# Kernel optimization log

Measured on AMD Instinct MI355X. Metric: run time of the kernel, lower is better.

Reference implementation:

```python
import jax, jax.numpy as jnp
import numpy as np

HEADS, KDIM, VDIM = 8, 32, 64  # ImageLinearAttention defaults
EPS = 1e-8

def lrelu(x):
    return jax.nn.leaky_relu(x, 0.2)

def up2(x):
    # torch nn.Upsample(scale_factor=2, mode='bilinear', align_corners=False)
    b, c, h, w = x.shape
    return jax.image.resize(x, (b, c, 2 * h, 2 * w), method='bilinear')

def blur(x):
    # normalized [1,2,1] outer-product depthwise blur (kornia filter2d, normalized=True)
    c = x.shape[1]
    f = jnp.array([1.0, 2.0, 1.0], dtype=x.dtype)
    k = (f[:, None] * f[None, :]) / 16.0
    kern = jnp.broadcast_to(k, (c, 1, 3, 3))
    return jax.lax.conv_general_dilated(x, kern, (1, 1), [(1, 1), (1, 1)], feature_group_count=c)

def conv2dmod(x, W, y, demod):
    # x [b,ci,h,w], W [co,ci,k,k], y [b,ci]; per-sample modulated (de)conv
    w = W[None] * (y[:, None, :, None, None] + 1.0)  # [b,co,ci,k,k]
    if demod:
        d = jax.lax.rsqrt(jnp.sum(w * w, axis=(2, 3, 4), keepdims=True) + EPS)
        w = w * d
    pad = (W.shape[-1] - 1) // 2  # same padding, stride=1, dilation=1
    conv1 = lambda xi, wi: jax.lax.conv_general_dilated(xi[None], wi, (1, 1), [(pad, pad), (pad, pad)])[0]
    return jax.vmap(conv1)(x, w)

def attn_and_ff(x, qw, kw, vw, ow, ob, ga, f1w, f1b, f2w, f2b, gf):
    # Residual(Rezero(ImageLinearAttention)) then Residual(Rezero(conv1x1-leaky-conv1x1))
    b, c, h, w = x.shape
    n = h * w
    xf = x.reshape(b, c, n)
    scale = KDIM ** -0.25
    q = (jnp.einsum('dc,bcn->bdn', qw, xf) * scale).reshape(b, HEADS, KDIM, n)
    k = (jnp.einsum('dc,bcn->bdn', kw, xf) * scale).reshape(b, HEADS, KDIM, n)
    v = jnp.einsum('dc,bcn->bdn', vw, xf).reshape(b, HEADS, VDIM, n)
    k = jax.nn.softmax(k, axis=-1)          # over pixels
    q = jax.nn.softmax(q, axis=-2)          # norm_queries: over key dim
    ctx = jnp.einsum('bhdn,bhen->bhde', k, v)
    out = jnp.einsum('bhdn,bhde->bhen', q, ctx).reshape(b, HEADS * VDIM, n)
    out = jnp.einsum('cd,bdn->bcn', ow, out) + ob[None, :, None]
    x = x + ga * out.reshape(b, c, h, w)
    h1 = lrelu(jnp.einsum('dc,bcn->bdn', f1w, x.reshape(b, c, n)) + f1b[None, :, None])
    ff = jnp.einsum('cd,bdn->bcn', f2w, h1) + f2b[None, :, None]
    return x + gf * ff.reshape(b, c, h, w)

def setup_inputs() -> dict:
    key = jax.random.key(0)
    ks = jax.random.split(key, 20)
    B, CIN, F, L, H, W = 4, 128, 64, 512, 64, 64
    DK, DV = HEADS * KDIM, HEADS * VDIM
    d = {}
    d['x'] = jax.random.normal(ks[0], (B, CIN, H, W), jnp.float32)
    d['prev_rgb'] = jax.random.normal(ks[1], (B, 3, 2 * H, 2 * W), jnp.float32)
    d['istyle'] = jax.random.normal(ks[2], (B, L), jnp.float32)
    d['noise1'] = jax.random.normal(ks[3], (B, F, 2 * H, 2 * W), jnp.float32)
    d['noise2'] = jax.random.normal(ks[4], (B, F, 2 * H, 2 * W), jnp.float32)
    d['conv1_w'] = jax.random.normal(ks[5], (F, CIN, 3, 3), jnp.float32) * (2.0 / (CIN * 9)) ** 0.5
    d['conv2_w'] = jax.random.normal(ks[6], (F, F, 3, 3), jnp.float32) * (2.0 / (F * 9)) ** 0.5
    d['style_w'] = jax.random.normal(ks[7], (F, L), jnp.float32) * L ** -0.5
    d['style_b'] = jnp.zeros((F,), jnp.float32)
    d['rgb_w'] = jax.random.normal(ks[8], (3, F, 1, 1), jnp.float32) * (2.0 / F) ** 0.5
    d['qw'] = jax.random.normal(ks[9], (2, DK, F), jnp.float32) * F ** -0.5
    d['kw'] = jax.random.normal(ks[10], (2, DK, F), jnp.float32) * F ** -0.5
    d['vw'] = jax.random.normal(ks[11], (2, DV, F), jnp.float32) * F ** -0.5
    d['ow'] = jax.random.normal(ks[12], (2, F, DV), jnp.float32) * DV ** -0.5
    d['ob'] = jnp.zeros((2, F), jnp.float32)
    d['ga'] = 0.1 * jnp.ones((2,), jnp.float32)  # rezero gate (nonzero for a meaningful baseline)
    d['f1w'] = jax.random.normal(ks[13], (2, 2 * F, F), jnp.float32) * F ** -0.5
    d['f1b'] = jnp.zeros((2, 2 * F), jnp.float32)
    d['f2w'] = jax.random.normal(ks[14], (2, F, 2 * F), jnp.float32) * (2 * F) ** -0.5
    d['f2b'] = jnp.zeros((2, F), jnp.float32)
    d['gf'] = 0.1 * jnp.ones((2,), jnp.float32)
    return d

def reference(x, prev_rgb, istyle, noise1, noise2, conv1_w, conv2_w, style_w, style_b, rgb_w,
              qw, kw, vw, ow, ob, ga, f1w, f1b, f2w, f2b, gf):
    b = x.shape[0]
    x = up2(x)
    n1 = attn_and_ff(noise1, qw[0], kw[0], vw[0], ow[0], ob[0], ga[0], f1w[0], f1b[0], f2w[0], f2b[0], gf[0])
    n2 = attn_and_ff(noise2, qw[1], kw[1], vw[1], ow[1], ob[1], ga[1], f1w[1], f1b[1], f2w[1], f2b[1], gf[1])
    ones1 = jnp.ones((b, conv1_w.shape[1]), x.dtype)  # style1 = ones
    x = lrelu(conv2dmod(x, conv1_w, ones1, True) + n1)
    ones2 = jnp.ones((b, conv2_w.shape[1]), x.dtype)  # style2 = ones
    x = lrelu(conv2dmod(x, conv2_w, ones2, True) + n2)
    style = istyle @ style_w.T + style_b             # RGBBlock.to_style
    rgb = conv2dmod(x, rgb_w, style, False) + prev_rgb
    rgb = blur(up2(rgb))                             # upsample_rgb: bilinear x2 + blur
    return (x, rgb)
```

## Files before the change

### kernel.cpp

```cpp
#include <hip/hip_runtime.h>
#include <math.h>

#define NB 4
#define NF 64
#define NPIX 16384
#define DK 256
#define DV 512
#define QKSCALE 0.4204482f

typedef __attribute__((ext_vector_type(8))) short bf16x8;
typedef __attribute__((ext_vector_type(4))) float f32x4;
#define MFMA16(a, b, c) __builtin_amdgcn_mfma_f32_16x16x32_bf16(a, b, c, 0, 0, 0)

__device__ __forceinline__ short f2bf(float f) {
  __bf16 h = (__bf16)f;
  return __builtin_bit_cast(short, h);
}
__device__ __forceinline__ float bf2f(short s) {
  unsigned u = ((unsigned)(unsigned short)s) << 16;
  return __builtin_bit_cast(float, u);
}

#define OFF_XUPT   0L
#define OFF_XAT    4194304L
#define OFF_NBT    6291456L
#define OFF_NZT    10485760L
#define OFF_GPART  14680064L
#define OFF_WB1    25165824L
#define OFF_WB2    25202688L
#define OFF_STYLE  25221120L
#define OFF_RGBS   25221376L
#define OFF_QWB    25417984L
#define OFF_KWB    25434368L
#define OFF_F1WB   25450752L
#define OFF_F2WB   25458944L
#define OFF_MTT    25467136L
#define OFF_GSUM   25532672L

#define CDIV(a,b) (((a)+(b)-1)/(b))

__global__ void cvt4_kernel(const float* __restrict__ qw, const float* __restrict__ kw,
                            const float* __restrict__ f1w, const float* __restrict__ f2w,
                            short* __restrict__ qwP, short* __restrict__ kwP,
                            short* __restrict__ f1P, short* __restrict__ f2P) {
  int i = blockIdx.x * 256 + threadIdx.x;
  if (i < 32768) {
    int i_t = i >> 14, rem = i & 16383;
    int hd = rem >> 10, ks = (rem >> 9) & 1, lane = (rem >> 3) & 63, j = rem & 7;
    int l15 = lane & 15, quad = lane >> 4;
    qwP[i] = f2bf(qw[i_t * 16384 + (hd * 16 + l15) * 64 + ks * 32 + quad * 8 + j]);
  } else if (i < 65536) {
    int ii = i - 32768;
    int i_t = ii >> 14, rem = ii & 16383;
    int q = rem >> 12, dt = (rem >> 10) & 3, ks = (rem >> 9) & 1, lane = (rem >> 3) & 63, j = rem & 7;
    int l15 = lane & 15, quad = lane >> 4;
    kwP[ii] = f2bf(kw[i_t * 16384 + (q * 64 + dt * 16 + l15) * 64 + ks * 32 + quad * 8 + j]);
  } else if (i < 81920) {
    int ii = i - 65536;
    int i_t = ii >> 13, rem = ii & 8191;
    int jt = rem >> 10, ks = (rem >> 9) & 1, lane = (rem >> 3) & 63, j = rem & 7;
    int l15 = lane & 15, quad = lane >> 4;
    f1P[ii] = f2bf(f1w[i_t * 8192 + (jt * 16 + l15) * 64 + ks * 32 + quad * 8 + j]);
  } else {
    int ii = i - 81920;
    int i_t = ii >> 13, rem = ii & 8191;
    int ct = rem >> 11, p = (rem >> 10) & 1, ks = (rem >> 9) & 1, lane = (rem >> 3) & 63, j = rem & 7;
    int l15 = lane & 15, quad = lane >> 4;
    f2P[ii] = f2bf(f2w[i_t * 8192 + (ct * 16 + l15) * 128 + p * 64 + ks * 32 + quad * 8 + j]);
  }
}

__global__ __launch_bounds__(256) void up2t_kernel(const float* __restrict__ in,
                                                   short* __restrict__ outT) {
  __shared__ float row[64 * 132];
  int b = blockIdx.y, y = blockIdx.x, tid = threadIdx.x;
  float iy = y * 0.5f - 0.25f;
  int y0 = (int)floorf(iy); float wy = iy - (float)y0;
  int ylo = y0 < 0 ? 0 : y0;
  int yhi = y0 + 1 > 63 ? 63 : y0 + 1;
  for (int it = 0; it < 32; ++it) {
    int idx = it * 256 + tid;
    int c = idx >> 6, xin = idx & 63;
    const float* bp = in + ((long)(b * 128 + c)) * 4096;
    float v0 = bp[ylo * 64 + xin];
    float v1 = bp[yhi * 64 + xin];
    row[xin * 132 + c] = (1.f - wy) * v0 + wy * v1;
  }
  __syncthreads();
  int x = tid >> 1, c0 = (tid & 1) * 64;
  float ix = x * 0.5f - 0.25f;
  int x0 = (int)floorf(ix); float wx = ix - (float)x0;
  int xlo = x0 < 0 ? 0 : x0;
  int xhi = x0 + 1 > 63 ? 63 : x0 + 1;
  long obase = (((long)(b * 128 + y)) * 128 + x) * 128 + c0;
#pragma unroll
  for (int i = 0; i < 8; ++i) {
    bf16x8 pack;
#pragma unroll
    for (int r = 0; r < 8; ++r) {
      int c = c0 + i * 8 + r;
      float v = (1.f - wx) * row[xlo * 132 + c] + wx * row[xhi * 132 + c];
      pack[r] = f2bf(v);
    }
    *(bf16x8*)(outT + obase + i * 8) = pack;
  }
}

__global__ __launch_bounds__(256) void nzt_kernel(const float* __restrict__ nz1,
                                                  const float* __restrict__ nz2,
                                                  short* __restrict__ nzP) {
  __shared__ short tile[64 * 65];
  int i = blockIdx.z, b = blockIdx.y;
  long n0 = (long)blockIdx.x * 64;
  const float* nz = (i == 0) ? nz1 : nz2;
  int tid = threadIdx.x;
  const float* src = nz + (long)b * 64 * NPIX + n0;
#pragma unroll
  for (int k = 0; k < 16; ++k) {
    int idx = tid + k * 256;
    int n = idx & 63, c = idx >> 6;
    tile[c * 65 + n] = f2bf(src[(long)c * NPIX + n]);
  }
  __syncthreads();
  long fragb = ((long)(i * NB + b)) * 1024 + blockIdx.x * 4;
#pragma unroll
  for (int v = 0; v < 2; ++v) {
    int vid = tid + v * 256;
    int ntl = vid >> 7, ks = (vid >> 6) & 1, lane = vid & 63;
    int l15 = lane & 15, quad = lane >> 4;
    bf16x8 pack;
#pragma unroll
    for (int j = 0; j < 8; ++j)
      pack[j] = tile[(ks * 32 + quad * 8 + j) * 65 + ntl * 16 + l15];
    *(bf16x8*)(nzP + ((fragb + ntl) * 2 + ks) * 512 + lane * 8) = pack;
  }
}

__global__ void wnormT_kernel(const float* __restrict__ W, short* __restrict__ wbP, int CI) {
  int co = blockIdx.x;
  int n = CI * 9;
  int KS = CI >> 5;
  __shared__ float red[256];
  float s = 0.f;
  for (int idx = threadIdx.x; idx < n; idx += 256) {
    float w2 = 2.0f * W[co * n + idx];
    s += w2 * w2;
  }
  red[threadIdx.x] = s;
  __syncthreads();
  for (int off = 128; off > 0; off >>= 1) {
    if (threadIdx.x < off) red[threadIdx.x] += red[threadIdx.x + off];
    __syncthreads();
  }
  float sc = rsqrtf(red[0] + 1e-8f);
  int ct = co >> 4, l15 = co & 15;
  for (int idx = threadIdx.x; idx < n; idx += 256) {
    int ci = idx / 9, k = idx - ci * 9;
    int ks = ci >> 5, quad = (ci >> 3) & 3, j = ci & 7;
    wbP[((k * 4 + ct) * KS + ks) * 512 + (quad * 16 + l15) * 8 + j] =
        f2bf(2.0f * W[co * n + idx] * sc);
  }
}

__global__ void style_kernel(const float* __restrict__ istyle, const float* __restrict__ sw,
                             const float* __restrict__ sb, float* __restrict__ styleb) {
  int b = threadIdx.x >> 6;
  int c = threadIdx.x & 63;
  float a = 0.f;
  const float* ip = istyle + b * 512;
  const float* wp = sw + c * 512;
  for (int l = 0; l < 512; ++l) a += ip[l] * wp[l];
  styleb[b * 64 + c] = a + sb[c];
}

__global__ __launch_bounds__(256, 4) void pk_kernel(const float* __restrict__ nz1,
                                                    const float* __restrict__ nz2,
                                                    const short* __restrict__ nzP,
                                                    const short* __restrict__ kwP,
                                                    short* __restrict__ Gpartb) {
  __shared__ __attribute__((aligned(16))) char lds[39168];
  int bi = blockIdx.x, ch = blockIdx.y;
  int i = bi >> 2, b = bi & 3;
  const float* nz = (i == 0) ? nz1 : nz2;
  const short* kwP_i = kwP + i * (DK * NF);
  int tid = threadIdx.x;
  int w = tid >> 6, lane = tid & 63, quad = lane >> 4, l15 = lane & 15;
  int n0 = ch * 128;
  short* Xb = (short*)lds;
  short* Ph = (short*)(lds + 21760);
  for (int k = 0; k < 32; ++k) {
    int idx = tid + k * 256;
    int c = idx >> 7, n = idx & 127;
    Xb[c * 136 + n] = f2bf(nz[((long)b * 64 + c) * NPIX + n0 + n]);
  }
  for (int k = 0; k < 8; ++k) {
    int idx = tid + k * 256;
    int c = 64 + (idx >> 7), n = idx & 127;
    Xb[c * 136 + n] = (c == 64) ? (short)0x3F80 : (short)0;
  }
  bf16x8 bfr[2][2];
#pragma unroll
  for (int j = 0; j < 2; ++j)
#pragma unroll
    for (int ks = 0; ks < 2; ++ks)
      bfr[j][ks] = *(const bf16x8*)(nzP +
          (((long)bi * 1024 + ch * 8 + 2 * w + j) * 2 + ks) * 512 + lane * 8);
  __syncthreads();
  for (int q = 0; q < 4; ++q) {
    f32x4 acc[2][4];
#pragma unroll
    for (int j = 0; j < 2; ++j)
#pragma unroll
      for (int dt = 0; dt < 4; ++dt) acc[j][dt] = (f32x4){0.f, 0.f, 0.f, 0.f};
#pragma unroll
    for (int j = 0; j < 2; ++j) {
#pragma unroll
      for (int ks = 0; ks < 2; ++ks) {
#pragma unroll
        for (int dt = 0; dt < 4; ++dt) {
          bf16x8 afr = *(const bf16x8*)(kwP_i + (((q * 4 + dt) * 2 + ks) * 512 + lane * 8));
          acc[j][dt] = MFMA16(afr, bfr[j][ks], acc[j][dt]);
        }
      }
    }
#pragma unroll
    for (int j = 0; j < 2; ++j) {
      int ntile = 2 * w + j;
#pragma unroll
      for (int dt = 0; dt < 4; ++dt)
#pragma unroll
        for (int r = 0; r < 4; ++r) {
          float p = __expf(acc[j][dt][r] * QKSCALE);
          Ph[(dt * 16 + quad * 4 + r) * 136 + ntile * 16 + l15] = f2bf(p);
        }
    }
    __syncthreads();
#pragma unroll
    for (int ct = 0; ct < 5; ++ct) {
      f32x4 g = (f32x4){0.f, 0.f, 0.f, 0.f};
#pragma unroll
      for (int ks = 0; ks < 4; ++ks) {
        bf16x8 afr = *(const bf16x8*)(Ph + (w * 16 + l15) * 136 + ks * 32 + quad * 8);
        bf16x8 bfr2 = *(const bf16x8*)(Xb + (ct * 16 + l15) * 136 + ks * 32 + quad * 8);
        g = MFMA16(afr, bfr2, g);
      }
#pragma unroll
      for (int r = 0; r < 4; ++r) {
        int row = q * 64 + w * 16 + quad * 4 + r;
        Gpartb[(((long)bi * 128 + ch) * 256 + row) * 80 + ct * 16 + l15] = f2bf(g[r]);
      }
    }
    __syncthreads();
  }
}

__global__ __launch_bounds__(256) void gsum_kernel(const short* __restrict__ Gpartb,
                                                   float* __restrict__ Gsum) {
  long idx = (long)blockIdx.x * 256 + threadIdx.x;
  int bi = (int)(idx / 20480);
  int rem = (int)(idx % 20480);
  const short* gp = Gpartb + (long)bi * 128 * 20480 + rem;
  float s = 0.f;
#pragma unroll 8
  for (int ch = 0; ch < 128; ++ch) s += bf2f(gp[(long)ch * 20480]);
  Gsum[idx] = s;
}

__global__ __launch_bounds__(256) void ctxM_kernel(const float* __restrict__ Gsum,
                                                   const float* __restrict__ vw,
                                                   const float* __restrict__ ow,
                                                   short* __restrict__ MtP) {
  int i = blockIdx.z, b = blockIdx.y, dt = blockIdx.x * 16;
  int h = dt >> 5;
  __shared__ float Gs[16][81];
  __shared__ float ctxs[16][68];
  int t = threadIdx.x;
  const float* gsb = Gsum + ((long)(i * NB + b)) * 20480;
  for (int idx = t; idx < 1280; idx += 256) {
    int dl = idx / 80, c = idx - dl * 80;
    Gs[dl][c] = gsb[(dt + dl) * 80 + c];
  }
  __syncthreads();
  const float* vw_i = vw + (long)i * DV * NF;
  const float* ow_i = ow + (long)i * NF * DV;
  for (int idx = t; idx < 1024; idx += 256) {
    int dl = idx & 15, e = idx >> 4;
    const float* vp = vw_i + (h * 64 + e) * 64;
    float a = 0.f;
#pragma unroll
    for (int c = 0; c < 64; ++c) a += Gs[dl][c] * vp[c];
    ctxs[dl][e] = a / Gs[dl][64];
  }
  __syncthreads();
  short* mtp = MtP + ((long)(i * NB + b)) * 16384;
  for (int idx = t; idx < 1024; idx += 256) {
    int dl = idx & 15, c = idx >> 4;
    const float* op = ow_i + c * 512 + h * 64;
    float a = 0.f;
#pragma unroll
    for (int e = 0; e < 64; ++e) a += op[e] * ctxs[dl][e];
    int d = dt + dl;
    int ct = c >> 4, l15 = c & 15, hh = d >> 5, quad = (d >> 3) & 3, r = d & 7;
    mtp[((ct * 8 + hh) * 64 + quad * 16 + l15) * 8 + r] = f2bf(a);
  }
}

__global__ __launch_bounds__(256, 8) void attnd4_kernel(
    const short* __restrict__ nzP, const short* __restrict__ qwP,
    const short* __restrict__ MtP, const float* __restrict__ ob,
    const float* __restrict__ gap, const short* __restrict__ f1P,
    const float* __restrict__ f1b, const short* __restrict__ f2P,
    const float* __restrict__ f2b, const float* __restrict__ gfp,
    short* __restrict__ noutP) {
  __shared__ __attribute__((aligned(16))) short lds[4 * 2048];
  int bi = blockIdx.x;
  int i = bi >> 2;
  int tid = threadIdx.x;
  int w = tid >> 6, lane = tid & 63, quad = lane >> 4, l15 = lane & 15;
  short* Xt = lds + w * 2048;
  short* Es = Xt + 1152;
  float ga = gap[i], gf = gfp[i];
  const short* qwP_i = qwP + i * (DK * NF);
  const short* f1P_i = f1P + i * (128 * 64);
  const float* f1b_i = f1b + i * 128;
  const short* f2P_i = f2P + i * (64 * 128);
  const float* f2b_i = f2b + i * 64;
  const float* ob_i = ob + i * 64;
  long ntile = (long)bi * 1024 + blockIdx.y * 4 + w;
  const short* nb = nzP + ntile * 1024;
  bf16x8 xfr0 = *(const bf16x8*)(nb + lane * 8);
  bf16x8 xfr1 = *(const bf16x8*)(nb + 512 + lane * 8);
  *(bf16x8*)(Xt + l15 * 72 + quad * 8) = xfr0;
  *(bf16x8*)(Xt + l15 * 72 + 32 + quad * 8) = xfr1;
  const short* mtp = MtP + (long)bi * 16384;
  f32x4 acc2[4];
#pragma unroll
  for (int ct = 0; ct < 4; ++ct) acc2[ct] = (f32x4){0.f, 0.f, 0.f, 0.f};
#pragma unroll
  for (int h = 0; h < 8; ++h) {
    f32x4 q[2];
#pragma unroll
    for (int dd = 0; dd < 2; ++dd) {
      int hd = 2 * h + dd;
      q[dd] = (f32x4){0.f, 0.f, 0.f, 0.f};
      bf16x8 a0 = *(const bf16x8*)(qwP_i + (hd * 2 + 0) * 512 + lane * 8);
      q[dd] = MFMA16(a0, xfr0, q[dd]);
      bf16x8 a1 = *(const bf16x8*)(qwP_i + (hd * 2 + 1) * 512 + lane * 8);
      q[dd] = MFMA16(a1, xfr1, q[dd]);
    }
    float part = 0.f;
#pragma unroll
    for (int dd = 0; dd < 2; ++dd)
#pragma unroll
      for (int r = 0; r < 4; ++r) {
        float e = __expf(q[dd][r] * QKSCALE);
        q[dd][r] = e;
        part += e;
      }
    float p2 = part + __shfl_xor(part, 16);
    float s = p2 + __shfl_xor(p2, 32);
    float inv = 1.0f / s;
#pragma unroll
    for (int dd = 0; dd < 2; ++dd) {
      short4 ev;
      ev.x = f2bf(q[dd][0] * inv); ev.y = f2bf(q[dd][1] * inv);
      ev.z = f2bf(q[dd][2] * inv); ev.w = f2bf(q[dd][3] * inv);
      *(short4*)(Es + l15 * 56 + dd * 16 + quad * 4) = ev;
    }
    bf16x8 efr = *(const bf16x8*)(Es + l15 * 56 + quad * 8);
#pragma unroll
    for (int ct = 0; ct < 4; ++ct) {
      bf16x8 afr = *(const bf16x8*)(mtp + (ct * 8 + h) * 512 + lane * 8);
      acc2[ct] = MFMA16(afr, efr, acc2[ct]);
    }
  }
  float yreg[4][4];
#pragma unroll
  for (int ct = 0; ct < 4; ++ct) {
    int c0 = ct * 16 + quad * 4;
    short4 xs = *(const short4*)(Xt + l15 * 72 + c0);
    float xv[4] = {bf2f(xs.x), bf2f(xs.y), bf2f(xs.z), bf2f(xs.w)};
    short4 ys;
#pragma unroll
    for (int r = 0; r < 4; ++r) yreg[ct][r] = xv[r] + ga * (acc2[ct][r] + ob_i[c0 + r]);
    ys.x = f2bf(yreg[ct][0]); ys.y = f2bf(yreg[ct][1]);
    ys.z = f2bf(yreg[ct][2]); ys.w = f2bf(yreg[ct][3]);
    *(short4*)(Xt + l15 * 72 + c0) = ys;
  }
  bf16x8 yfr0 = *(const bf16x8*)(Xt + l15 * 72 + quad * 8);
  bf16x8 yfr1 = *(const bf16x8*)(Xt + l15 * 72 + 32 + quad * 8);
  f32x4 acc3[8];
#pragma unroll
  for (int jt = 0; jt < 8; ++jt) {
    acc3[jt] = (f32x4){0.f, 0.f, 0.f, 0.f};
    bf16x8 a0 = *(const bf16x8*)(f1P_i + (jt * 2 + 0) * 512 + lane * 8);
    acc3[jt] = MFMA16(a0, yfr0, acc3[jt]);
    bf16x8 a1 = *(const bf16x8*)(f1P_i + (jt * 2 + 1) * 512 + lane * 8);
    acc3[jt] = MFMA16(a1, yfr1, acc3[jt]);
  }
  f32x4 acc4[4];
#pragma unroll
  for (int ct = 0; ct < 4; ++ct) acc4[ct] = (f32x4){0.f, 0.f, 0.f, 0.f};
#pragma unroll
  for (int p = 0; p < 2; ++p) {
#pragma unroll
    for (int jj = 0; jj < 4; ++jj) {
      int jt = p * 4 + jj;
      short4 hs;
#pragma unroll
      for (int r = 0; r < 4; ++r) {
        float a = acc3[jt][r] + f1b_i[jt * 16 + quad * 4 + r];
        a = a > 0.f ? a : 0.2f * a;
        ((short*)&hs)[r] = f2bf(a);
      }
      *(short4*)(Xt + l15 * 72 + jj * 16 + quad * 4) = hs;
    }
    bf16x8 h0 = *(const bf16x8*)(Xt + l15 * 72 + quad * 8);
    bf16x8 h1 = *(const bf16x8*)(Xt + l15 * 72 + 32 + quad * 8);
#pragma unroll
    for (int ct = 0; ct < 4; ++ct) {
      bf16x8 a0 = *(const bf16x8*)(f2P_i + ((ct * 2 + p) * 2 + 0) * 512 + lane * 8);
      acc4[ct] = MFMA16(a0, h0, acc4[ct]);
      bf16x8 a1 = *(const bf16x8*)(f2P_i + ((ct * 2 + p) * 2 + 1) * 512 + lane * 8);
      acc4[ct] = MFMA16(a1, h1, acc4[ct]);
    }
  }
#pragma unroll
  for (int ct = 0; ct < 4; ++ct) {
    int c0 = ct * 16 + quad * 4;
    short4 ov;
#pragma unroll
    for (int r = 0; r < 4; ++r)
      ((short*)&ov)[r] = f2bf(yreg[ct][r] + gf * (acc4[ct][r] + f2b_i[c0 + r]));
    *(short4*)(noutP + (ntile * 4 + ct) * 256 + lane * 4) = ov;
  }
}

__global__ __launch_bounds__(256, 4) void convmfma_kernel(
    const short* __restrict__ inT, int CI, const short* __restrict__ wbP,
    const short* __restrict__ addnP, float* __restrict__ out_nchw,
    short* __restrict__ out_nhwc, const float* __restrict__ rgbw,
    const float* __restrict__ styleb, const float* __restrict__ prev,
    float* __restrict__ rgbs) {
  __shared__ __attribute__((aligned(16))) short Bs[3 * 66 * 40];
  int xh = blockIdx.x, y = blockIdx.y, b = blockIdx.z;
  int tid = threadIdx.x;
  int w = tid >> 6, lane = tid & 63, quad = lane >> 4, l15 = lane & 15;
  int KS = CI >> 5;
  f32x4 acc[4];
#pragma unroll
  for (int ct = 0; ct < 4; ++ct) acc[ct] = (f32x4){0.f, 0.f, 0.f, 0.f};
  for (int ks = 0; ks < KS; ++ks) {
    if (ks) __syncthreads();
    for (int t = tid; t < 792; t += 256) {
      int ci8 = t & 3, xr = t >> 2;
      int xi = xr % 66, r = xr / 66;
      int gy = y + r - 1, gx = xh * 64 + xi - 1;
      bf16x8 v = {0, 0, 0, 0, 0, 0, 0, 0};
      if (gy >= 0 && gy < 128 && gx >= 0 && gx < 128)
        v = *(const bf16x8*)(inT + (((long)(b * 128 + gy)) * 128 + gx) * CI + ks * 32 + ci8 * 8);
      *(bf16x8*)(Bs + (r * 66 + xi) * 40 + ci8 * 8) = v;
    }
    __syncthreads();
#pragma unroll
    for (int sh = 0; sh < 9; ++sh) {
      int dyv = sh / 3, dxv = sh - dyv * 3;
      const short* wbase = wbP + ((sh * 4) * KS + ks) * 512 + lane * 8;
      bf16x8 a0 = *(const bf16x8*)(wbase);
      bf16x8 a1 = *(const bf16x8*)(wbase + KS * 512);
      bf16x8 a2 = *(const bf16x8*)(wbase + 2 * KS * 512);
      bf16x8 a3 = *(const bf16x8*)(wbase + 3 * KS * 512);
      int xi = w * 16 + l15 + dxv;
      bf16x8 bf = *(const bf16x8*)(Bs + (dyv * 66 + xi) * 40 + quad * 8);
      acc[0] = MFMA16(a0, bf, acc[0]);
      acc[1] = MFMA16(a1, bf, acc[1]);
      acc[2] = MFMA16(a2, bf, acc[2]);
      acc[3] = MFMA16(a3, bf, acc[3]);
    }
  }
  int x = xh * 64 + w * 16 + l15;
  long nidx = ((long)(b * 128 + y)) * 128 + x;
  long ntile = (long)b * 1024 + y * 8 + xh * 4 + w;
  float p0 = 0.f, p1 = 0.f, p2 = 0.f;
#pragma unroll
  for (int ct = 0; ct < 4; ++ct) {
    short4 ad = *(const short4*)(addnP + (ntile * 4 + ct) * 256 + lane * 4);
    float av[4] = {bf2f(ad.x), bf2f(ad.y), bf2f(ad.z), bf2f(ad.w)};
    float v[4];
#pragma unroll
    for (int r = 0; r < 4; ++r) {
      float a = acc[ct][r] + av[r];
      v[r] = a > 0.f ? a : 0.2f * a;
    }
    if (out_nchw) {
#pragma unroll
      for (int r = 0; r < 4; ++r) {
        int co = ct * 16 + quad * 4 + r;
        out_nchw[((long)(b * 64 + co)) * 16384 + y * 128 + x] = v[r];
      }
    }
    if (out_nhwc) {
      short4 pv;
      pv.x = f2bf(v[0]); pv.y = f2bf(v[1]); pv.z = f2bf(v[2]); pv.w = f2bf(v[3]);
      *(short4*)(out_nhwc + nidx * 64 + ct * 16 + quad * 4) = pv;
    }
    if (rgbw) {
#pragma unroll
      for (int r = 0; r < 4; ++r) {
        int co = ct * 16 + quad * 4 + r;
        float mv = (styleb[b * 64 + co] + 1.0f) * v[r];
        p0 += rgbw[co] * mv;
        p1 += rgbw[64 + co] * mv;
        p2 += rgbw[128 + co] * mv;
      }
    }
  }
  if (rgbw) {
    p0 += __shfl_xor(p0, 16); p0 += __shfl_xor(p0, 32);
    p1 += __shfl_xor(p1, 16); p1 += __shfl_xor(p1, 32);
    p2 += __shfl_xor(p2, 16); p2 += __shfl_xor(p2, 32);
    if (quad == 0) {
      long pi = y * 128 + x;
      rgbs[((long)(b * 3 + 0)) * 16384 + pi] = p0 + prev[((long)(b * 3 + 0)) * 16384 + pi];
      rgbs[((long)(b * 3 + 1)) * 16384 + pi] = p1 + prev[((long)(b * 3 + 1)) * 16384 + pi];
      rgbs[((long)(b * 3 + 2)) * 16384 + pi] = p2 + prev[((long)(b * 3 + 2)) * 16384 + pi];
    }
  }
}

__global__ void upblur_kernel(const float* __restrict__ rgbs, float* __restrict__ out) {
  __shared__ float rows[3][128];
  int bc = blockIdx.y, Y = blockIdx.x, X = threadIdx.x;
  int m = Y >> 1;
  const float* base = rgbs + (long)bc * 16384;
  for (int t = X; t < 384; t += 256) {
    int sr = t >> 7, xx = t & 127;
    int rr = m - 1 + sr;
    rr = rr < 0 ? 0 : (rr > 127 ? 127 : rr);
    rows[sr][xx] = base[rr * 128 + xx];
  }
  __syncthreads();
  const float w3[3] = {1.f, 2.f, 1.f};
  float s = 0.f;
#pragma unroll
  for (int dy = -1; dy <= 1; ++dy) {
    int Yv = Y + dy;
    if (Yv < 0 || Yv > 255) continue;
    float iy = Yv * 0.5f - 0.25f;
    int y0 = (int)floorf(iy); float wy = iy - (float)y0;
    int ylo = y0 < 0 ? 0 : y0;
    int yhi = y0 + 1 > 127 ? 127 : y0 + 1;
    int slo = ylo - m + 1, shi = yhi - m + 1;
#pragma unroll
    for (int dx = -1; dx <= 1; ++dx) {
      int Xv = X + dx;
      if (Xv < 0 || Xv > 255) continue;
      float ix = Xv * 0.5f - 0.25f;
      int x0 = (int)floorf(ix); float wx = ix - (float)x0;
      int xlo = x0 < 0 ? 0 : x0;
      int xhi = x0 + 1 > 127 ? 127 : x0 + 1;
      float v = (1.f - wy) * ((1.f - wx) * rows[slo][xlo] + wx * rows[slo][xhi])
              + wy * ((1.f - wx) * rows[shi][xlo] + wx * rows[shi][xhi]);
      s += w3[dy + 1] * w3[dx + 1] * v;
    }
  }
  out[(long)bc * 65536 + Y * 256 + X] = s * (1.0f / 16.0f);
}

extern "C" void kernel_launch(void* const* d_in, const int* in_sizes, int n_in,
                              void* d_out, int out_size, void* d_ws, size_t ws_size,
                              hipStream_t stream) {
  (void)in_sizes; (void)n_in; (void)out_size; (void)ws_size;
  const float* x        = (const float*)d_in[0];
  const float* prev_rgb = (const float*)d_in[1];
  const float* istyle   = (const float*)d_in[2];
  const float* noise1   = (const float*)d_in[3];
  const float* noise2   = (const float*)d_in[4];
  const float* conv1_w  = (const float*)d_in[5];
  const float* conv2_w  = (const float*)d_in[6];
  const float* style_w  = (const float*)d_in[7];
  const float* style_b  = (const float*)d_in[8];
  const float* rgb_w    = (const float*)d_in[9];
  const float* qw       = (const float*)d_in[10];
  const float* kw       = (const float*)d_in[11];
  const float* vw       = (const float*)d_in[12];
  const float* ow       = (const float*)d_in[13];
  const float* ob       = (const float*)d_in[14];
  const float* ga       = (const float*)d_in[15];
  const float* f1w      = (const float*)d_in[16];
  const float* f1b      = (const float*)d_in[17];
  const float* f2w      = (const float*)d_in[18];
  const float* f2b      = (const float*)d_in[19];
  const float* gf       = (const float*)d_in[20];
  float* out_x   = (float*)d_out;
  float* out_rgb = out_x + 4194304;
  float* ws = (float*)d_ws;

  short* xupT   = (short*)(ws + OFF_XUPT);
  short* xaT    = (short*)(ws + OFF_XAT);
  short* nbufP  = (short*)(ws + OFF_NBT);
  short* nzP    = (short*)(ws + OFF_NZT);
  short* Gpartb = (short*)(ws + OFF_GPART);
  short* wb1    = (short*)(ws + OFF_WB1);
  short* wb2    = (short*)(ws + OFF_WB2);
  float* styleb = ws + OFF_STYLE;
  float* rgbs   = ws + OFF_RGBS;
  short* qwP    = (short*)(ws + OFF_QWB);
  short* kwP    = (short*)(ws + OFF_KWB);
  short* f1P    = (short*)(ws + OFF_F1WB);
  short* f2P    = (short*)(ws + OFF_F2WB);
  short* MtP    = (short*)(ws + OFF_MTT);
  float* Gsum   = ws + OFF_GSUM;

  cvt4_kernel<<<384, 256, 0, stream>>>(qw, kw, f1w, f2w, qwP, kwP, f1P, f2P);
  wnormT_kernel<<<64, 256, 0, stream>>>(conv1_w, wb1, 128);
  wnormT_kernel<<<64, 256, 0, stream>>>(conv2_w, wb2, 64);
  style_kernel<<<1, 256, 0, stream>>>(istyle, style_w, style_b, styleb);
  up2t_kernel<<<dim3(128, NB), 256, 0, stream>>>(x, xupT);
  nzt_kernel<<<dim3(256, NB, 2), 256, 0, stream>>>(noise1, noise2, nzP);

  pk_kernel<<<dim3(8, 128), 256, 0, stream>>>(noise1, noise2, nzP, kwP, Gpartb);
  gsum_kernel<<<640, 256, 0, stream>>>(Gpartb, Gsum);
  ctxM_kernel<<<dim3(16, NB, 2), 256, 0, stream>>>(Gsum, vw, ow, MtP);
  attnd4_kernel<<<dim3(8, 256), 256, 0, stream>>>(nzP, qwP, MtP, ob, ga,
                                                  f1P, f1b, f2P, f2b, gf, nbufP);

  convmfma_kernel<<<dim3(2, 128, NB), 256, 0, stream>>>(
      xupT, 128, wb1, nbufP, nullptr, xaT, nullptr, nullptr, nullptr, nullptr);
  convmfma_kernel<<<dim3(2, 128, NB), 256, 0, stream>>>(
      xaT, 64, wb2, nbufP + 4194304L, out_x, nullptr, rgb_w, styleb, prev_rgb, rgbs);

  upblur_kernel<<<dim3(256, 12), 256, 0, stream>>>(rgbs, out_rgb);
}
```

Baseline: 307.3 us.

## Merge small prep kernels, remap upsample-transpose writes, relax attention launch bounds

The style projection is folded into an extra block of the weight-conversion kernel, and the two weight-normalization launches become one kernel covering both convs, which removes several tiny launches. The upsample-transpose kernel's output mapping changes so that each group of 16 lanes writes one contiguous 128-channel pixel row, improving write coalescing. The attention kernel's launch bound drops from 8 to 6 blocks per CU, which allows more registers per thread at the cost of lower occupancy.

```diff
diff --git a/kernel.cpp b/kernel.cpp
--- a/kernel.cpp
+++ b/kernel.cpp
@@ -42,7 +42,19 @@
 __global__ void cvt4_kernel(const float* __restrict__ qw, const float* __restrict__ kw,
                             const float* __restrict__ f1w, const float* __restrict__ f2w,
                             short* __restrict__ qwP, short* __restrict__ kwP,
-                            short* __restrict__ f1P, short* __restrict__ f2P) {
+                            short* __restrict__ f1P, short* __restrict__ f2P,
+                            const float* __restrict__ istyle, const float* __restrict__ sw,
+                            const float* __restrict__ sb, float* __restrict__ styleb) {
+  if (blockIdx.x == 384) {
+    int b = threadIdx.x >> 6;
+    int c = threadIdx.x & 63;
+    float a = 0.f;
+    const float* ip = istyle + b * 512;
+    const float* wp = sw + c * 512;
+    for (int l = 0; l < 512; ++l) a += ip[l] * wp[l];
+    styleb[b * 64 + c] = a + sb[c];
+    return;
+  }
   int i = blockIdx.x * 256 + threadIdx.x;
   if (i < 32768) {
     int i_t = i >> 14, rem = i & 16383;
@@ -74,6 +86,7 @@
                                                    short* __restrict__ outT) {
   __shared__ float row[64 * 132];
   int b = blockIdx.y, y = blockIdx.x, tid = threadIdx.x;
+  int w = tid >> 6, lane = tid & 63, quad = lane >> 4, l15 = lane & 15;
   float iy = y * 0.5f - 0.25f;
   int y0 = (int)floorf(iy); float wy = iy - (float)y0;
   int ylo = y0 < 0 ? 0 : y0;
@@ -87,22 +100,22 @@
     row[xin * 132 + c] = (1.f - wy) * v0 + wy * v1;
   }
   __syncthreads();
-  int x = tid >> 1, c0 = (tid & 1) * 64;
-  float ix = x * 0.5f - 0.25f;
-  int x0 = (int)floorf(ix); float wx = ix - (float)x0;
-  int xlo = x0 < 0 ? 0 : x0;
-  int xhi = x0 + 1 > 63 ? 63 : x0 + 1;
-  long obase = (((long)(b * 128 + y)) * 128 + x) * 128 + c0;
-#pragma unroll
-  for (int i = 0; i < 8; ++i) {
+  long ybase = (((long)(b * 128 + y)) * 128) * 128;
+#pragma unroll
+  for (int s = 0; s < 8; ++s) {
+    int x = w * 32 + s * 4 + quad;
+    float ix = x * 0.5f - 0.25f;
+    int x0 = (int)floorf(ix); float wx = ix - (float)x0;
+    int xlo = x0 < 0 ? 0 : x0;
+    int xhi = x0 + 1 > 63 ? 63 : x0 + 1;
     bf16x8 pack;
 #pragma unroll
-    for (int r = 0; r < 8; ++r) {
-      int c = c0 + i * 8 + r;
+    for (int j = 0; j < 8; ++j) {
+      int c = l15 * 8 + j;
       float v = (1.f - wx) * row[xlo * 132 + c] + wx * row[xhi * 132 + c];
-      pack[r] = f2bf(v);
-    }
-    *(bf16x8*)(outT + obase + i * 8) = pack;
+      pack[j] = f2bf(v);
+    }
+    *(bf16x8*)(outT + ybase + (long)x * 128 + l15 * 8) = pack;
   }
 }
 
@@ -136,8 +149,13 @@
   }
 }
 
-__global__ void wnormT_kernel(const float* __restrict__ W, short* __restrict__ wbP, int CI) {
-  int co = blockIdx.x;
+__global__ void wnorm2_kernel(const float* __restrict__ W1, const float* __restrict__ W2,
+                              short* __restrict__ wb1, short* __restrict__ wb2) {
+  int which = blockIdx.x >> 6;
+  int co = blockIdx.x & 63;
+  const float* W = which ? W2 : W1;
+  short* wbP = which ? wb2 : wb1;
+  int CI = which ? 64 : 128;
   int n = CI * 9;
   int KS = CI >> 5;
   __shared__ float red[256];
@@ -160,17 +178,6 @@
     wbP[((k * 4 + ct) * KS + ks) * 512 + (quad * 16 + l15) * 8 + j] =
         f2bf(2.0f * W[co * n + idx] * sc);
   }
-}
-
-__global__ void style_kernel(const float* __restrict__ istyle, const float* __restrict__ sw,
-                             const float* __restrict__ sb, float* __restrict__ styleb) {
-  int b = threadIdx.x >> 6;
-  int c = threadIdx.x & 63;
-  float a = 0.f;
-  const float* ip = istyle + b * 512;
-  const float* wp = sw + c * 512;
-  for (int l = 0; l < 512; ++l) a += ip[l] * wp[l];
-  styleb[b * 64 + c] = a + sb[c];
 }
 
 __global__ __launch_bounds__(256, 4) void pk_kernel(const float* __restrict__ nz1,
@@ -305,7 +312,7 @@
   }
 }
 
-__global__ __launch_bounds__(256, 8) void attnd4_kernel(
+__global__ __launch_bounds__(256, 6) void attnd4_kernel(
     const short* __restrict__ nzP, const short* __restrict__ qwP,
     const short* __restrict__ MtP, const float* __restrict__ ob,
     const float* __restrict__ gap, const short* __restrict__ f1P,
@@ -612,10 +619,9 @@
   short* MtP    = (short*)(ws + OFF_MTT);
   float* Gsum   = ws + OFF_GSUM;
 
-  cvt4_kernel<<<384, 256, 0, stream>>>(qw, kw, f1w, f2w, qwP, kwP, f1P, f2P);
-  wnormT_kernel<<<64, 256, 0, stream>>>(conv1_w, wb1, 128);
-  wnormT_kernel<<<64, 256, 0, stream>>>(conv2_w, wb2, 64);
-  style_kernel<<<1, 256, 0, stream>>>(istyle, style_w, style_b, styleb);
+  cvt4_kernel<<<385, 256, 0, stream>>>(qw, kw, f1w, f2w, qwP, kwP, f1P, f2P,
+                                       istyle, style_w, style_b, styleb);
+  wnorm2_kernel<<<128, 256, 0, stream>>>(conv1_w, conv2_w, wb1, wb2);
   up2t_kernel<<<dim3(128, NB), 256, 0, stream>>>(x, xupT);
   nzt_kernel<<<dim3(256, NB, 2), 256, 0, stream>>>(noise1, noise2, nzP);
 
```

Result: faster. 294.4 us (-4.2%).
